# Performance work log

Hardware: AMD Instinct MI355X
Metric: run time of the kernel (lower is better)

## Reference

```python
import jax, jax.numpy as jnp
import numpy as np

N_HEAD = 16

def setup_inputs() -> dict:
    key = jax.random.key(0)
    ks = jax.random.split(key, 4)
    C = 2048
    x = jax.random.normal(ks[0], (4, 2048, C), dtype=jnp.float32)
    # weights stored [in, out] (transpose of torch Linear's [out, in]); same math y = x @ W + b
    w_qkv = jax.random.normal(ks[1], (C, 3 * C), dtype=jnp.float32) * (1.0 / np.sqrt(C))
    b_qkv = jnp.zeros((3 * C,), dtype=jnp.float32)
    w_proj = jax.random.normal(ks[2], (C, C), dtype=jnp.float32) * (1.0 / np.sqrt(C))
    b_proj = jnp.zeros((C,), dtype=jnp.float32)
    return {"x": x, "w_qkv": w_qkv, "b_qkv": b_qkv, "w_proj": w_proj, "b_proj": b_proj}

def reference(x, w_qkv, b_qkv, w_proj, b_proj):
    B, S, C = x.shape
    H = N_HEAD
    D = C // H
    qkv = x @ w_qkv + b_qkv                      # [B,S,3C]
    q, k, v = jnp.split(qkv, 3, axis=-1)
    # [B,H,S,D]
    q = q.reshape(B, S, H, D).transpose(0, 2, 1, 3)
    k = k.reshape(B, S, H, D).transpose(0, 2, 1, 3)
    v = v.reshape(B, S, H, D).transpose(0, 2, 1, 3)
    scale = 1.0 / np.sqrt(D).astype(np.float32)
    scores = jnp.einsum('bhqd,bhkd->bhqk', q, k) * scale   # [B,H,S,S]
    causal = jnp.tril(jnp.ones((S, S), dtype=bool))
    scores = jnp.where(causal, scores, jnp.finfo(scores.dtype).min)
    attn = jax.nn.softmax(scores, axis=-1)
    y = jnp.einsum('bhqk,bhkd->bhqd', attn, v)              # [B,H,S,D]
    y = y.transpose(0, 2, 1, 3).reshape(B, S, C)
    return y @ w_proj + b_proj
```

## Files before the change

kernel.cpp:

```cpp
#include <hip/hip_runtime.h>
#include <hip/hip_bf16.h>

typedef __bf16 bf16x8 __attribute__((ext_vector_type(8)));
typedef float floatx4 __attribute__((ext_vector_type(4)));

#define LDK 72

__device__ __forceinline__ unsigned short f2bf(float f) {
  unsigned u = __float_as_uint(f);
  u += 0x7fffu + ((u >> 16) & 1u);
  return (unsigned short)(u >> 16);
}

__device__ __forceinline__ void async_copy16(const void* g, void* l) {
  __builtin_amdgcn_global_load_lds(
      (const __attribute__((address_space(1))) void*)g,
      (__attribute__((address_space(3))) void*)l, 16, 0, 0);
}

__global__ __launch_bounds__(256) void cvt_bf16(
    const float* __restrict__ in, unsigned short* __restrict__ out) {
  size_t i = ((size_t)blockIdx.x * 256 + threadIdx.x) * 8;
  float4 a0 = *(const float4*)&in[i];
  float4 a1 = *(const float4*)&in[i + 4];
  uint4 d;
  d.x = (unsigned)f2bf(a0.x) | ((unsigned)f2bf(a0.y) << 16);
  d.y = (unsigned)f2bf(a0.z) | ((unsigned)f2bf(a0.w) << 16);
  d.z = (unsigned)f2bf(a1.x) | ((unsigned)f2bf(a1.y) << 16);
  d.w = (unsigned)f2bf(a1.z) | ((unsigned)f2bf(a1.w) << 16);
  *(uint4*)(&out[i]) = d;
}

__global__ __launch_bounds__(256) void transpose_cvt(
    const float* __restrict__ in, unsigned short* __restrict__ out,
    int R, int Ccol) {
  __shared__ unsigned short tile[32][33];
  int c0 = blockIdx.x * 32, r0 = blockIdx.y * 32;
  int tx = threadIdx.x & 31, ty = threadIdx.x >> 5;
  #pragma unroll
  for (int i = 0; i < 32; i += 8)
    tile[ty + i][tx] = f2bf(in[(size_t)(r0 + ty + i) * Ccol + c0 + tx]);
  __syncthreads();
  #pragma unroll
  for (int i = 0; i < 32; i += 8)
    out[(size_t)(c0 + ty + i) * R + r0 + tx] = tile[tx][ty + i];
}

__device__ __forceinline__ void gemm_bt_mainloop(
    const unsigned short* __restrict__ A, const unsigned short* __restrict__ Bt,
    int K, int m0, int n0,
    unsigned short* As, unsigned short* Bs, floatx4 acc[4][4]) {
  const int t = threadIdx.x;
  const int lane = t & 63, w = t >> 6;
  const int wm = w >> 1, wn = w & 1;
  const int l15 = lane & 15, l4 = lane >> 4;
  const int lrow = lane >> 3, lchunk = lane & 7;
  const int gch = lchunk ^ lrow;
  const floatx4 zf = {0.f, 0.f, 0.f, 0.f};
  #pragma unroll
  for (int mi = 0; mi < 4; mi++)
    #pragma unroll
    for (int ni = 0; ni < 4; ni++) acc[mi][ni] = zf;

  for (int k0 = 0; k0 < K; k0 += 64) {
    __syncthreads();
    #pragma unroll
    for (int i = 0; i < 4; i++) {
      int ridx = w * 4 + i;
      int row = ridx * 8 + lrow;
      async_copy16(&A[(size_t)(m0 + row) * K + k0 + gch * 8], &As[ridx * 512]);
    }
    #pragma unroll
    for (int i = 0; i < 4; i++) {
      int ridx = w * 4 + i;
      int row = ridx * 8 + lrow;
      async_copy16(&Bt[(size_t)(n0 + row) * K + k0 + gch * 8], &Bs[ridx * 512]);
    }
    __syncthreads();
    #pragma unroll
    for (int kk = 0; kk < 2; kk++) {
      bf16x8 af[4], bfr[4];
      #pragma unroll
      for (int mi = 0; mi < 4; mi++) {
        int row = wm * 64 + mi * 16 + l15;
        af[mi] = *(const bf16x8*)(&As[row * 64 + ((kk * 4 + l4) ^ (l15 & 7)) * 8]);
      }
      #pragma unroll
      for (int ni = 0; ni < 4; ni++) {
        int row = wn * 64 + ni * 16 + l15;
        bfr[ni] = *(const bf16x8*)(&Bs[row * 64 + ((kk * 4 + l4) ^ (l15 & 7)) * 8]);
      }
      #pragma unroll
      for (int mi = 0; mi < 4; mi++)
        #pragma unroll
        for (int ni = 0; ni < 4; ni++)
          acc[mi][ni] = __builtin_amdgcn_mfma_f32_16x16x32_bf16(
              af[mi], bfr[ni], acc[mi][ni], 0, 0, 0);
    }
  }
}

__global__ __launch_bounds__(256, 3) void gemm_qkv(
    const unsigned short* __restrict__ X, const unsigned short* __restrict__ WT,
    const float* __restrict__ bias,
    unsigned short* __restrict__ Qo, unsigned short* __restrict__ Ko,
    unsigned short* __restrict__ Vto) {
  __shared__ unsigned short As[128 * 64];
  __shared__ unsigned short Bs[128 * 64];
  int n0 = blockIdx.x * 128, m0 = blockIdx.y * 128;
  floatx4 acc[4][4];
  gemm_bt_mainloop(X, WT, 2048, m0, n0, As, Bs, acc);

  const int t = threadIdx.x, lane = t & 63, w = t >> 6;
  const int wm = w >> 1, wn = w & 1;
  const int l15 = lane & 15, l4 = lane >> 4;
  int which = n0 >> 11;
  int h = (n0 & 2047) >> 7;
  int b = m0 >> 11;
  int s0 = m0 & 2047;
  float bv[4];
  #pragma unroll
  for (int ni = 0; ni < 4; ni++)
    bv[ni] = bias[n0 + wn * 64 + ni * 16 + l15];

  if (which < 2) {
    unsigned short* dst = (which == 0) ? Qo : Ko;
    size_t base = (size_t)(b * 16 + h) * 2048;
    #pragma unroll
    for (int mi = 0; mi < 4; mi++)
      #pragma unroll
      for (int ni = 0; ni < 4; ni++) {
        int d = wn * 64 + ni * 16 + l15;
        #pragma unroll
        for (int r = 0; r < 4; r++) {
          int srow = s0 + wm * 64 + mi * 16 + l4 * 4 + r;
          dst[(base + srow) * 128 + d] = f2bf(acc[mi][ni][r] + bv[ni]);
        }
      }
  } else {
    #pragma unroll
    for (int mi = 0; mi < 4; mi++)
      #pragma unroll
      for (int ni = 0; ni < 4; ni++) {
        int d = wn * 64 + ni * 16 + l15;
        int sr = s0 + wm * 64 + mi * 16 + l4 * 4;
        ushort4 v;
        v.x = f2bf(acc[mi][ni][0] + bv[ni]);
        v.y = f2bf(acc[mi][ni][1] + bv[ni]);
        v.z = f2bf(acc[mi][ni][2] + bv[ni]);
        v.w = f2bf(acc[mi][ni][3] + bv[ni]);
        *(ushort4*)(&Vto[((size_t)(b * 16 + h) * 128 + d) * 2048 + sr]) = v;
      }
  }
}

__device__ __forceinline__ void attn_stage(
    const unsigned short* __restrict__ Kb, const unsigned short* __restrict__ Vb,
    __bf16* Ksel, __bf16* Vsel, int k0, int lane, int w) {
  const int krow_in = lane >> 4, kch = lane & 15;
  const int vrow_in = lane >> 3, vch = lane & 7;
  #pragma unroll
  for (int u = 0; u < 4; u++) {
    int uk = w * 4 + u;
    int row = uk * 4 + krow_in;
    int sch = kch ^ (row & 7);
    async_copy16(&Kb[(size_t)(k0 + row) * 128 + sch * 8], Ksel + uk * 512);
  }
  #pragma unroll
  for (int u = 0; u < 4; u++) {
    int uv = w * 4 + u;
    int row = uv * 8 + vrow_in;
    int sch = vch ^ vrow_in;
    async_copy16(&Vb[(size_t)row * 2048 + k0 + sch * 8], Vsel + uv * 512);
  }
}

__global__ __launch_bounds__(256, 2) void attn(
    const unsigned short* __restrict__ Qg, const unsigned short* __restrict__ Kg,
    const unsigned short* __restrict__ Vtg, unsigned short* __restrict__ Yg) {
  const int S = 2048, Dh = 128;
  const float c1 = 0.08838834764831845f * 1.4426950408889634f;
  const float NEG_BIG = -3.0e38f;
  __shared__ __bf16 Ks[2][64 * 128];
  __shared__ __bf16 Vs[2][128 * 64];
  __shared__ __bf16 Pl[4][16 * LDK];

  int wg = blockIdx.x;
  int lg = (wg & 7) * 128 + (wg >> 3);
  int qtp = lg & 15;
  int bh = lg >> 4;
  const int t = threadIdx.x, lane = t & 63, w = t >> 6;
  const int l15 = lane & 15, l4 = lane >> 4;
  const unsigned short* Qb = Qg + (size_t)bh * S * Dh;
  const unsigned short* Kb = Kg + (size_t)bh * S * Dh;
  const unsigned short* Vb = Vtg + (size_t)bh * Dh * S;
  __bf16* Pw = Pl[w];
  int b = bh >> 4, h = bh & 15;
  const floatx4 zf = {0.f, 0.f, 0.f, 0.f};

  #pragma unroll 1
  for (int half = 0; half < 2; half++) {
    int qt = half ? qtp : (31 - qtp);
    int q0 = qt * 64;
    int qrow_base = q0 + w * 16;
    bf16x8 qf[4];
    #pragma unroll
    for (int kk = 0; kk < 4; kk++)
      qf[kk] = *(const bf16x8*)(
          &Qb[(size_t)(qrow_base + l15) * Dh + kk * 32 + l4 * 8]);
    floatx4 accO[8];
    #pragma unroll
    for (int nd = 0; nd < 8; nd++) accO[nd] = zf;
    float mst[4], lst[4];
    #pragma unroll
    for (int r = 0; r < 4; r++) { mst[r] = NEG_BIG; lst[r] = 0.f; }

    int ntiles = qt + 1;
    int cur = 0;
    attn_stage(Kb, Vb, Ks[0], Vs[0], 0, lane, w);
    __syncthreads();

    #pragma unroll 1
    for (int kt = 0; kt < ntiles; kt++) {
      if (kt + 1 < ntiles)
        attn_stage(Kb, Vb, Ks[cur ^ 1], Vs[cur ^ 1], (kt + 1) * 64, lane, w);

      const __bf16* Kcur = Ks[cur];
      const __bf16* Vcur = Vs[cur];
      floatx4 sc[4];
      #pragma unroll
      for (int ni = 0; ni < 4; ni++) sc[ni] = zf;
      #pragma unroll
      for (int kk = 0; kk < 4; kk++) {
        bf16x8 kf[4];
        #pragma unroll
        for (int ni = 0; ni < 4; ni++) {
          int row = ni * 16 + l15;
          kf[ni] = *(const bf16x8*)(
              &Kcur[row * 128 + (((kk * 4 + l4) ^ (l15 & 7)) << 3)]);
        }
        #pragma unroll
        for (int ni = 0; ni < 4; ni++)
          sc[ni] = __builtin_amdgcn_mfma_f32_16x16x32_bf16(qf[kk], kf[ni], sc[ni], 0, 0, 0);
      }

      if (kt == qt) {
        #pragma unroll
        for (int ni = 0; ni < 4; ni++)
          #pragma unroll
          for (int r = 0; r < 4; r++)
            if (ni * 16 + l15 > w * 16 + l4 * 4 + r) sc[ni][r] = NEG_BIG;
      }
      float mt[4];
      #pragma unroll
      for (int r = 0; r < 4; r++)
        mt[r] = fmaxf(fmaxf(sc[0][r], sc[1][r]), fmaxf(sc[2][r], sc[3][r]));
      #pragma unroll
      for (int off = 1; off < 16; off <<= 1)
        #pragma unroll
        for (int r = 0; r < 4; r++)
          mt[r] = fmaxf(mt[r], __shfl_xor(mt[r], off, 64));
      float alpha[4], rs[4];
      #pragma unroll
      for (int r = 0; r < 4; r++) {
        float mnew = fmaxf(mst[r], mt[r]);
        alpha[r] = exp2f((mst[r] - mnew) * c1);
        mst[r] = mnew;
        rs[r] = 0.f;
      }
      #pragma unroll
      for (int ni = 0; ni < 4; ni++)
        #pragma unroll
        for (int r = 0; r < 4; r++) {
          float p = exp2f((sc[ni][r] - mst[r]) * c1);
          rs[r] += p;
          Pw[(l4 * 4 + r) * LDK + ni * 16 + l15] = __builtin_bit_cast(__bf16, f2bf(p));
        }
      #pragma unroll
      for (int off = 1; off < 16; off <<= 1)
        #pragma unroll
        for (int r = 0; r < 4; r++)
          rs[r] += __shfl_xor(rs[r], off, 64);
      #pragma unroll
      for (int r = 0; r < 4; r++)
        lst[r] = lst[r] * alpha[r] + rs[r];
      #pragma unroll
      for (int nd = 0; nd < 8; nd++)
        #pragma unroll
        for (int r = 0; r < 4; r++) accO[nd][r] *= alpha[r];
      #pragma unroll
      for (int kk = 0; kk < 2; kk++) {
        bf16x8 pf = *(const bf16x8*)(&Pw[l15 * LDK + kk * 32 + l4 * 8]);
        #pragma unroll
        for (int nd = 0; nd < 8; nd++) {
          int row = nd * 16 + l15;
          bf16x8 vf = *(const bf16x8*)(
              &Vcur[row * 64 + (((kk * 4 + l4) ^ (l15 & 7)) << 3)]);
          accO[nd] = __builtin_amdgcn_mfma_f32_16x16x32_bf16(pf, vf, accO[nd], 0, 0, 0);
        }
      }
      __syncthreads();
      cur ^= 1;
    }
    #pragma unroll
    for (int r = 0; r < 4; r++) {
      float inv = 1.0f / lst[r];
      int srow = qrow_base + l4 * 4 + r;
      size_t rowbase = ((size_t)(b * 2048 + srow)) * 2048 + h * 128;
      #pragma unroll
      for (int nd = 0; nd < 8; nd++)
        Yg[rowbase + nd * 16 + l15] = f2bf(accO[nd][r] * inv);
    }
  }
}

__global__ __launch_bounds__(256, 3) void gemm_proj(
    const unsigned short* __restrict__ Yin, const unsigned short* __restrict__ WT,
    const float* __restrict__ bias, float* __restrict__ Og) {
  __shared__ unsigned short As[128 * 64];
  __shared__ unsigned short Bs[128 * 64];
  int n0 = blockIdx.x * 128, m0 = blockIdx.y * 128;
  floatx4 acc[4][4];
  gemm_bt_mainloop(Yin, WT, 2048, m0, n0, As, Bs, acc);

  const int t = threadIdx.x, lane = t & 63, w = t >> 6;
  const int wm = w >> 1, wn = w & 1;
  const int l15 = lane & 15, l4 = lane >> 4;
  float bv[4];
  #pragma unroll
  for (int ni = 0; ni < 4; ni++)
    bv[ni] = bias[n0 + wn * 64 + ni * 16 + l15];
  #pragma unroll
  for (int mi = 0; mi < 4; mi++)
    #pragma unroll
    for (int ni = 0; ni < 4; ni++)
      #pragma unroll
      for (int r = 0; r < 4; r++)
        Og[(size_t)(m0 + wm * 64 + mi * 16 + l4 * 4 + r) * 2048 +
           n0 + wn * 64 + ni * 16 + l15] = acc[mi][ni][r] + bv[ni];
}

extern "C" void kernel_launch(void* const* d_in, const int* in_sizes, int n_in,
                              void* d_out, int out_size, void* d_ws, size_t ws_size,
                              hipStream_t stream) {
  const float* x      = (const float*)d_in[0];
  const float* w_qkv  = (const float*)d_in[1];
  const float* b_qkv  = (const float*)d_in[2];
  const float* w_proj = (const float*)d_in[3];
  const float* b_proj = (const float*)d_in[4];
  float* out = (float*)d_out;
  char* ws = (char*)d_ws;

  unsigned short* Q   = (unsigned short*)d_out;
  unsigned short* Kt  = (unsigned short*)((char*)d_out + 33554432);
  unsigned short* Vt  = (unsigned short*)(ws);
  unsigned short* Xbf = (unsigned short*)(ws + 33554432);
  unsigned short* Y   = (unsigned short*)(ws + 33554432);
  unsigned short* WqT = (unsigned short*)(ws + 67108864);
  unsigned short* WpT = (unsigned short*)(ws + 67108864);

  cvt_bf16<<<dim3(8192), 256, 0, stream>>>(x, Xbf);
  transpose_cvt<<<dim3(192, 64), 256, 0, stream>>>(w_qkv, WqT, 2048, 6144);
  gemm_qkv<<<dim3(48, 64), 256, 0, stream>>>(Xbf, WqT, b_qkv, Q, Kt, Vt);
  attn<<<dim3(1024), 256, 0, stream>>>(Q, Kt, Vt, Y);
  transpose_cvt<<<dim3(64, 64), 256, 0, stream>>>(w_proj, WpT, 2048, 2048);
  gemm_proj<<<dim3(16, 64), 256, 0, stream>>>(Y, WpT, b_proj, out);
}
```

Before: 626.7 us.

## Rework attention into 128-row query blocks with transposed scores and lazy rescaling

The attention kernel now uses 512-thread blocks of 8 waves covering 128 query rows, so each staged K/V tile is shared by twice as many waves and each thread issues half the async copies. The score MFMA is transposed so each lane owns one query row. That turns the per-row max and sum into two cross-lane shuffles and allows a single-scalar online-softmax state. Rescaling of the output accumulator is skipped when the running max grows by no more than a threshold, P is packed with v_cvt_pk_bf16 into a swizzled LDS layout, and s_setprio is raised around the MFMA sections. In exchange, causal tiles near the diagonal do more masked work, block-level sync spans more waves, and the lazy-rescale threshold loosens numeric bounds somewhat.

```diff
diff --git a/kernel.cpp b/kernel.cpp
--- a/kernel.cpp
+++ b/kernel.cpp
@@ -3,13 +3,17 @@
 
 typedef __bf16 bf16x8 __attribute__((ext_vector_type(8)));
 typedef float floatx4 __attribute__((ext_vector_type(4)));
-
-#define LDK 72
 
 __device__ __forceinline__ unsigned short f2bf(float f) {
   unsigned u = __float_as_uint(f);
   u += 0x7fffu + ((u >> 16) & 1u);
   return (unsigned short)(u >> 16);
+}
+
+__device__ __forceinline__ unsigned cvt_pk_bf16(float lo, float hi) {
+  unsigned r;
+  asm("v_cvt_pk_bf16_f32 %0, %1, %2" : "=v"(r) : "v"(lo), "v"(hi));
+  return r;
 }
 
 __device__ __forceinline__ void async_copy16(const void* g, void* l) {
@@ -160,22 +164,22 @@
   const int krow_in = lane >> 4, kch = lane & 15;
   const int vrow_in = lane >> 3, vch = lane & 7;
   #pragma unroll
-  for (int u = 0; u < 4; u++) {
-    int uk = w * 4 + u;
+  for (int u = 0; u < 2; u++) {
+    int uk = w * 2 + u;
     int row = uk * 4 + krow_in;
     int sch = kch ^ (row & 7);
     async_copy16(&Kb[(size_t)(k0 + row) * 128 + sch * 8], Ksel + uk * 512);
   }
   #pragma unroll
-  for (int u = 0; u < 4; u++) {
-    int uv = w * 4 + u;
+  for (int u = 0; u < 2; u++) {
+    int uv = w * 2 + u;
     int row = uv * 8 + vrow_in;
     int sch = vch ^ vrow_in;
     async_copy16(&Vb[(size_t)row * 2048 + k0 + sch * 8], Vsel + uv * 512);
   }
 }
 
-__global__ __launch_bounds__(256, 2) void attn(
+__global__ __launch_bounds__(512, 4) void attn(
     const unsigned short* __restrict__ Qg, const unsigned short* __restrict__ Kg,
     const unsigned short* __restrict__ Vtg, unsigned short* __restrict__ Yg) {
   const int S = 2048, Dh = 128;
@@ -183,26 +187,26 @@
   const float NEG_BIG = -3.0e38f;
   __shared__ __bf16 Ks[2][64 * 128];
   __shared__ __bf16 Vs[2][128 * 64];
-  __shared__ __bf16 Pl[4][16 * LDK];
+  __shared__ __bf16 Ps[8][16 * 64];
 
   int wg = blockIdx.x;
-  int lg = (wg & 7) * 128 + (wg >> 3);
-  int qtp = lg & 15;
-  int bh = lg >> 4;
+  int lg = (wg & 7) * 64 + (wg >> 3);
+  int qtp = lg & 7;
+  int bh = lg >> 3;
   const int t = threadIdx.x, lane = t & 63, w = t >> 6;
   const int l15 = lane & 15, l4 = lane >> 4;
   const unsigned short* Qb = Qg + (size_t)bh * S * Dh;
   const unsigned short* Kb = Kg + (size_t)bh * S * Dh;
   const unsigned short* Vb = Vtg + (size_t)bh * Dh * S;
-  __bf16* Pw = Pl[w];
+  __bf16* Pw = Ps[w];
   int b = bh >> 4, h = bh & 15;
   const floatx4 zf = {0.f, 0.f, 0.f, 0.f};
 
   #pragma unroll 1
   for (int half = 0; half < 2; half++) {
-    int qt = half ? qtp : (31 - qtp);
-    int q0 = qt * 64;
-    int qrow_base = q0 + w * 16;
+    int jq = half ? qtp : (15 - qtp);
+    int qb0 = jq * 128;
+    int qrow_base = qb0 + w * 16;
     bf16x8 qf[4];
     #pragma unroll
     for (int kk = 0; kk < 4; kk++)
@@ -211,11 +215,9 @@
     floatx4 accO[8];
     #pragma unroll
     for (int nd = 0; nd < 8; nd++) accO[nd] = zf;
-    float mst[4], lst[4];
-    #pragma unroll
-    for (int r = 0; r < 4; r++) { mst[r] = NEG_BIG; lst[r] = 0.f; }
-
-    int ntiles = qt + 1;
+    float mst = NEG_BIG, lst = 0.f;
+
+    int ntiles = 2 * jq + 2;
     int cur = 0;
     attn_stage(Kb, Vb, Ks[0], Vs[0], 0, lane, w);
     __syncthreads();
@@ -230,6 +232,7 @@
       floatx4 sc[4];
       #pragma unroll
       for (int ni = 0; ni < 4; ni++) sc[ni] = zf;
+      __builtin_amdgcn_s_setprio(1);
       #pragma unroll
       for (int kk = 0; kk < 4; kk++) {
         bf16x8 kf[4];
@@ -241,56 +244,70 @@
         }
         #pragma unroll
         for (int ni = 0; ni < 4; ni++)
-          sc[ni] = __builtin_amdgcn_mfma_f32_16x16x32_bf16(qf[kk], kf[ni], sc[ni], 0, 0, 0);
-      }
-
-      if (kt == qt) {
+          sc[ni] = __builtin_amdgcn_mfma_f32_16x16x32_bf16(kf[ni], qf[kk], sc[ni], 0, 0, 0);
+      }
+      __builtin_amdgcn_s_setprio(0);
+
+      if (kt >= 2 * jq) {
+        int kb = kt * 64 - qb0 - w * 16 - l15;
         #pragma unroll
         for (int ni = 0; ni < 4; ni++)
           #pragma unroll
           for (int r = 0; r < 4; r++)
-            if (ni * 16 + l15 > w * 16 + l4 * 4 + r) sc[ni][r] = NEG_BIG;
-      }
-      float mt[4];
-      #pragma unroll
-      for (int r = 0; r < 4; r++)
-        mt[r] = fmaxf(fmaxf(sc[0][r], sc[1][r]), fmaxf(sc[2][r], sc[3][r]));
-      #pragma unroll
-      for (int off = 1; off < 16; off <<= 1)
+            if (kb + ni * 16 + l4 * 4 + r > 0) sc[ni][r] = NEG_BIG;
+      }
+
+      float mt = fmaxf(fmaxf(fmaxf(sc[0][0], sc[0][1]), fmaxf(sc[0][2], sc[0][3])),
+                       fmaxf(fmaxf(sc[1][0], sc[1][1]), fmaxf(sc[1][2], sc[1][3])));
+      mt = fmaxf(mt,
+           fmaxf(fmaxf(fmaxf(sc[2][0], sc[2][1]), fmaxf(sc[2][2], sc[2][3])),
+                 fmaxf(fmaxf(sc[3][0], sc[3][1]), fmaxf(sc[3][2], sc[3][3]))));
+      mt = fmaxf(mt, __shfl_xor(mt, 16, 64));
+      mt = fmaxf(mt, __shfl_xor(mt, 32, 64));
+
+      if (!__all(mt <= mst + 8.0f)) {
+        float mnew = fmaxf(mst, mt);
+        float alpha = exp2f((mst - mnew) * c1);
+        mst = mnew;
+        lst *= alpha;
+        float ar[4];
         #pragma unroll
         for (int r = 0; r < 4; r++)
-          mt[r] = fmaxf(mt[r], __shfl_xor(mt[r], off, 64));
-      float alpha[4], rs[4];
-      #pragma unroll
-      for (int r = 0; r < 4; r++) {
-        float mnew = fmaxf(mst[r], mt[r]);
-        alpha[r] = exp2f((mst[r] - mnew) * c1);
-        mst[r] = mnew;
-        rs[r] = 0.f;
-      }
+          ar[r] = __shfl(alpha, l4 * 20 + r, 64);
+        #pragma unroll
+        for (int nd = 0; nd < 8; nd++)
+          #pragma unroll
+          for (int r = 0; r < 4; r++) accO[nd][r] *= ar[r];
+      }
+
+      float mc = mst * c1;
+      float p[4][4];
+      float rs = 0.f;
       #pragma unroll
       for (int ni = 0; ni < 4; ni++)
         #pragma unroll
         for (int r = 0; r < 4; r++) {
-          float p = exp2f((sc[ni][r] - mst[r]) * c1);
-          rs[r] += p;
-          Pw[(l4 * 4 + r) * LDK + ni * 16 + l15] = __builtin_bit_cast(__bf16, f2bf(p));
+          p[ni][r] = exp2f(sc[ni][r] * c1 - mc);
+          rs += p[ni][r];
         }
-      #pragma unroll
-      for (int off = 1; off < 16; off <<= 1)
-        #pragma unroll
-        for (int r = 0; r < 4; r++)
-          rs[r] += __shfl_xor(rs[r], off, 64);
-      #pragma unroll
-      for (int r = 0; r < 4; r++)
-        lst[r] = lst[r] * alpha[r] + rs[r];
-      #pragma unroll
-      for (int nd = 0; nd < 8; nd++)
-        #pragma unroll
-        for (int r = 0; r < 4; r++) accO[nd][r] *= alpha[r];
+      rs += __shfl_xor(rs, 16, 64);
+      rs += __shfl_xor(rs, 32, 64);
+      lst += rs;
+
+      #pragma unroll
+      for (int ni = 0; ni < 4; ni++) {
+        uint2 dw;
+        dw.x = cvt_pk_bf16(p[ni][0], p[ni][1]);
+        dw.y = cvt_pk_bf16(p[ni][2], p[ni][3]);
+        int s = ni * 4 + l4;
+        *(uint2*)(&Pw[l15 * 64 + (((s >> 1) ^ (l15 & 7)) << 3) + ((s & 1) << 2)]) = dw;
+      }
+
+      __builtin_amdgcn_s_setprio(1);
       #pragma unroll
       for (int kk = 0; kk < 2; kk++) {
-        bf16x8 pf = *(const bf16x8*)(&Pw[l15 * LDK + kk * 32 + l4 * 8]);
+        bf16x8 pf = *(const bf16x8*)(
+            &Pw[l15 * 64 + (((kk * 4 + l4) ^ (l15 & 7)) << 3)]);
         #pragma unroll
         for (int nd = 0; nd < 8; nd++) {
           int row = nd * 16 + l15;
@@ -299,17 +316,23 @@
           accO[nd] = __builtin_amdgcn_mfma_f32_16x16x32_bf16(pf, vf, accO[nd], 0, 0, 0);
         }
       }
+      __builtin_amdgcn_s_setprio(0);
       __syncthreads();
       cur ^= 1;
     }
+
+    float invl = 1.0f / lst;
+    float ivr[4];
+    #pragma unroll
+    for (int r = 0; r < 4; r++)
+      ivr[r] = __shfl(invl, l4 * 20 + r, 64);
     #pragma unroll
     for (int r = 0; r < 4; r++) {
-      float inv = 1.0f / lst[r];
       int srow = qrow_base + l4 * 4 + r;
       size_t rowbase = ((size_t)(b * 2048 + srow)) * 2048 + h * 128;
       #pragma unroll
       for (int nd = 0; nd < 8; nd++)
-        Yg[rowbase + nd * 16 + l15] = f2bf(accO[nd][r] * inv);
+        Yg[rowbase + nd * 16 + l15] = f2bf(accO[nd][r] * ivr[r]);
     }
   }
 }
@@ -362,7 +385,7 @@
   cvt_bf16<<<dim3(8192), 256, 0, stream>>>(x, Xbf);
   transpose_cvt<<<dim3(192, 64), 256, 0, stream>>>(w_qkv, WqT, 2048, 6144);
   gemm_qkv<<<dim3(48, 64), 256, 0, stream>>>(Xbf, WqT, b_qkv, Q, Kt, Vt);
-  attn<<<dim3(1024), 256, 0, stream>>>(Q, Kt, Vt, Y);
+  attn<<<dim3(512), 512, 0, stream>>>(Q, Kt, Vt, Y);
   transpose_cvt<<<dim3(64, 64), 256, 0, stream>>>(w_proj, WpT, 2048, 2048);
   gemm_proj<<<dim3(16, 64), 256, 0, stream>>>(Y, WpT, b_proj, out);
 }
```

Result: faster. 565.2 us (-9.8%).
